# Kernel tuning notes

Hardware: AMD Instinct MI355X
Metric: run time of the kernel (lower is better)

## Reference

```python
import jax, jax.numpy as jnp
import numpy as np
from jax import lax

KS = 3
N = KS * KS  # 9 sampling locations per output pixel


def conv2d(x, w, b, pad, dil=1):
    out = lax.conv_general_dilated(
        x, w, window_strides=(1, 1), padding=((pad, pad), (pad, pad)),
        rhs_dilation=(dil, dil), dimension_numbers=('NCHW', 'OIHW', 'NCHW'))
    return out + b[None, :, None, None]


def deform_conv(x, p_w, p_b, dw, db):
    # Pure deform-conv-v2 semantics: offsets from p_conv, bilinear gather on
    # zero-padded input, then 3x3 contraction over the 9 gathered samples.
    B, C, H, W = x.shape
    offset = conv2d(x, p_w, p_b, 1)                       # (B, 2N, H, W)
    xp = jnp.pad(x, ((0, 0), (0, 0), (1, 1), (1, 1)))     # zero pad by 1
    Hp, Wp = H + 2, W + 2
    rr = jnp.arange(-(KS // 2), KS // 2 + 1)
    pi, pj = jnp.meshgrid(rr, rr, indexing='ij')
    p_n = jnp.concatenate([pi.reshape(-1), pj.reshape(-1)]).astype(x.dtype)   # (2N,)
    gi, gj = jnp.meshgrid(jnp.arange(1, H + 1), jnp.arange(1, W + 1), indexing='ij')
    p0 = jnp.concatenate([jnp.broadcast_to(gi, (N, H, W)),
                          jnp.broadcast_to(gj, (N, H, W))], 0).astype(x.dtype)  # (2N,H,W)
    p = p0[None] + p_n[None, :, None, None] + offset      # (B, 2N, H, W)
    p = jnp.transpose(p, (0, 2, 3, 1))                    # (B, H, W, 2N)
    py, px = p[..., :N], p[..., N:]
    fy, fx = jnp.floor(py), jnp.floor(px)
    lt_y = jnp.clip(fy, 0, Hp - 1); lt_x = jnp.clip(fx, 0, Wp - 1)
    rb_y = jnp.clip(fy + 1, 0, Hp - 1); rb_x = jnp.clip(fx + 1, 0, Wp - 1)
    pyc = jnp.clip(py, 0, Hp - 1); pxc = jnp.clip(px, 0, Wp - 1)
    g_lt = (1 + (lt_y - pyc)) * (1 + (lt_x - pxc))
    g_rb = (1 - (rb_y - pyc)) * (1 - (rb_x - pxc))
    g_lb = (1 + (lt_y - pyc)) * (1 - (rb_x - pxc))
    g_rt = (1 - (rb_y - pyc)) * (1 + (lt_x - pxc))
    xf = xp.reshape(B, C, Hp * Wp)

    def gather(qy, qx):
        idx = (qy.astype(jnp.int32) * Wp + qx.astype(jnp.int32)).reshape(B, -1)
        g = jax.vmap(lambda xb, ib: jnp.take(xb, ib, axis=1))(xf, idx)
        return g.reshape(B, C, H, W, N)

    x_lt = gather(lt_y, lt_x); x_rb = gather(rb_y, rb_x)
    x_lb = gather(lt_y, rb_x); x_rt = gather(rb_y, lt_x)
    samples = (g_lt[:, None] * x_lt + g_rb[:, None] * x_rb
               + g_lb[:, None] * x_lb + g_rt[:, None] * x_rt)  # (B,C,H,W,N)
    out = jnp.einsum('bchwn,ocn->bohw', samples, dw.reshape(dw.shape[0], C, N))
    return out + db[None, :, None, None]


def reference(x, w1, b1, w2, b2, w3, b3, w4, b4, p_w, p_b, dw, db, cw, cb):
    branches = [(w1, b1, 1, 1.0), (w2, b2, 3, 3.0), (w3, b3, 5, 5.0), (w4, b4, 7, 7.0)]
    feats = [deform_conv(conv2d(x, w, b, d, d) * s, p_w, p_b, dw, db)
             for (w, b, d, s) in branches]
    combined = jnp.concatenate(feats, axis=1)             # (B, 4*Cout, H, W)
    return jax.nn.relu(conv2d(combined, cw, cb, 0))


def setup_inputs() -> dict:
    B, Cin, Cout, H, W = 4, 128, 64, 128, 128
    key = jax.random.key(0)
    ks = jax.random.split(key, 16)
    sc3 = 1.0 / np.sqrt(Cin * 9)      # fan-in scale for 3x3 convs
    sc1 = 1.0 / np.sqrt(4 * Cout)     # fan-in scale for 1x1 fuse conv
    scd = 1.0 / np.sqrt(Cout * 9)     # deform main conv
    inp = {'x': jax.random.normal(ks[0], (B, Cin, H, W), jnp.float32)}
    for i in range(4):
        inp[f'w{i+1}'] = jax.random.normal(ks[1 + i], (Cout, Cin, 3, 3), jnp.float32) * sc3
        inp[f'b{i+1}'] = jax.random.normal(ks[5 + i], (Cout,), jnp.float32) * 0.01
    inp['p_w'] = jax.random.normal(ks[9], (2 * N, Cout, 3, 3), jnp.float32) * 0.01
    inp['p_b'] = jax.random.normal(ks[10], (2 * N,), jnp.float32) * 0.01
    inp['dw'] = jax.random.normal(ks[11], (Cout, Cout, 3, 3), jnp.float32) * scd
    inp['db'] = jax.random.normal(ks[12], (Cout,), jnp.float32) * 0.01
    inp['cw'] = jax.random.normal(ks[13], (Cout, 4 * Cout, 1, 1), jnp.float32) * sc1
    inp['cb'] = jax.random.normal(ks[14], (Cout,), jnp.float32) * 0.01
    return inp
```

## Files before the change

### kernel.cpp

```cpp
#include <hip/hip_runtime.h>
#include <hip/hip_fp16.h>

#define H 128
#define W 128
#define CIN 128
#define COUT 64
#define HW (H*W)
#define XW 130
#define FSL (XW*XW*64)
#define XTD 144

typedef __half f16;
typedef __attribute__((ext_vector_type(8)))  _Float16 h16x8;
typedef __attribute__((ext_vector_type(16))) float f32x16;

__device__ __forceinline__ float b2f(f16 v){ return __half2float(v); }
__device__ __forceinline__ f16  f2b(float v){ return __float2half_rn(v); }
__device__ __forceinline__ unsigned pack2(float a, float b){
    unsigned short ua = __builtin_bit_cast(unsigned short, f2b(a));
    unsigned short ub = __builtin_bit_cast(unsigned short, f2b(b));
    return (unsigned)ua | ((unsigned)ub << 16);
}
__device__ __forceinline__ unsigned short b16u(float v){
    return __builtin_bit_cast(unsigned short, f2b(v));
}
__device__ __forceinline__ __half2 uh2(unsigned u){
    return __builtin_bit_cast(__half2, u);
}
__device__ __forceinline__ unsigned h2u(__half2 v){
    return __builtin_bit_cast(unsigned, v);
}
__device__ __forceinline__ unsigned bcasth2(float v){
    __half h = __float2half_rn(v);
    return h2u(__halves2half2(h, h));
}
__device__ __forceinline__ void gld16(const void* g, void* l){
    __builtin_amdgcn_global_load_lds(
        (const __attribute__((address_space(1))) void*)g,
        (__attribute__((address_space(3))) void*)l, 16, 0, 0);
}

__global__ __launch_bounds__(256) void k_prep(
    const float* __restrict__ w1, const float* __restrict__ w2,
    const float* __restrict__ w3, const float* __restrict__ w4,
    const float* __restrict__ dw, const float* __restrict__ cw,
    const float* __restrict__ pw,
    uint4* __restrict__ xt4, unsigned* __restrict__ wbt,
    unsigned* __restrict__ dwb2, unsigned* __restrict__ cwb2,
    unsigned* __restrict__ pwb)
{
    int bid = blockIdx.x;
    int t = threadIdx.x;
    if (bid < 1024){
        const int n4 = (4*XTD*XTD*64)/4;
        for (int i = bid*256 + t; i < n4; i += 1024*256)
            xt4[i] = make_uint4(0,0,0,0);
    } else if (bid < 1600){
        int tid = (bid-1024)*256 + t;
        int cpl = tid & 7;
        int oc  = (tid >> 3) & 63;
        int tap = (tid >> 9) % 9;
        int cg  = (tid / 4608) & 7;
        int d   = tid / 36864;
        const float* wt = (d==0)?w1:(d==1)?w2:(d==2)?w3:w4;
        int c = cg*8 + cpl;
        wbt[tid] = pack2(wt[((size_t)oc*CIN + 2*c  )*9 + tap],
                         wt[((size_t)oc*CIN + 2*c+1)*9 + tap]);
    } else if (bid < 1672){
        int i = (bid-1600)*256 + t;
        int n = i>>11, oc = (i>>5)&63, cp = i&31;
        dwb2[i] = pack2(dw[((size_t)oc*64 + 2*cp  )*9 + n],
                        dw[((size_t)oc*64 + 2*cp+1)*9 + n]);
    } else if (bid < 1704){
        int i = (bid-1672)*256 + t;
        int kc = i>>9;
        int hf = (i>>8)&1;
        int oc = (i>>2)&63;
        int cl = i&3;
        int cp = kc*8 + hf*4 + cl;
        cwb2[i] = pack2(cw[(size_t)oc*256 + 2*cp], cw[(size_t)oc*256 + 2*cp+1]);
    } else {
        int i = (bid-1704)*256 + t;
        int cl = i & 3, oc = (i>>2)&31, hf = (i>>7)&1, cq = (i>>8)&3, tap = i>>10;
        int c = cq*16 + hf*8 + cl*2;
        unsigned v = 0u;
        if (oc < 18)
            v = pack2(pw[((size_t)oc*64 + c  )*9 + tap],
                      pw[((size_t)oc*64 + c+1)*9 + tap]);
        pwb[i] = v;
    }
}

__global__ __launch_bounds__(256) void k_xprep(
    const float* __restrict__ x, unsigned* __restrict__ xt)
{
    int y = blockIdx.x, b = blockIdx.y;
    int t = threadIdx.x;
    __shared__ float xsm[64*131];
    for (int ci0 = 0; ci0 < 128; ci0 += 64){
        for (int i=0;i<32;i++){
            int idx = t + 256*i;
            int col = idx & 127, ci = idx >> 7;
            xsm[ci*131 + col] = x[(((size_t)b*CIN + ci0+ci)*H + y)*W + col];
        }
        __syncthreads();
        for (int i=0;i<16;i++){
            int idx = t + 256*i;
            int cpg = idx & 31, col = idx >> 5;
            int cgg = (ci0 >> 4) + (cpg >> 3);
            int cpl = cpg & 7;
            unsigned u = pack2(xsm[(2*cpg)*131 + col], xsm[(2*cpg+1)*131 + col]);
            xt[((((size_t)b*8 + cgg)*XTD + y+8)*XTD + col+8)*8 + cpl] = u;
        }
        __syncthreads();
    }
}

__global__ __launch_bounds__(256,3) void k_branch_mfma(
    const unsigned* __restrict__ xt, const unsigned* __restrict__ wbt,
    const float* __restrict__ b1, const float* __restrict__ b2,
    const float* __restrict__ b3, const float* __restrict__ b4,
    f16* __restrict__ feats2)
{
    int bid = blockIdx.x;
    int xcd = bid & 7;
    int j   = bid >> 3;
    int zb  = xcd + 8*(j & 1);
    int hp  = j >> 1;
    int d = zb >> 2, b = zb & 3;
    int dil = 2*d + 1;
    int h0 = hp*2;
    const float* bs = (d==0)?b1:(d==1)?b2:(d==2)?b3:b4;
    const float scale = (float)dil;

    __shared__ unsigned smem[6912 + 4608];
    unsigned* As = smem;
    unsigned* Bs = smem + 6912;
    const unsigned short* As16 = (const unsigned short*)As;
    const unsigned short* Bs16 = (const unsigned short*)Bs;

    int t = threadIdx.x;
    int lane = t & 63;
    int w = t >> 6;
    int l31 = lane & 31;
    int half = lane >> 5;

    f16* fb = feats2 + (size_t)zb*FSL;
    if (t < 32){
        int yy = h0 + 1 + (t>>4);
        int side = (t>>3)&1;
        int q = t & 7;
        uint4 z = make_uint4(0,0,0,0);
        *(uint4*)((unsigned short*)fb + ((size_t)yy*XW + side*129)*64 + q*8) = z;
    }
    if (hp == 0){
        uint4 z = make_uint4(0,0,0,0);
        for (int i=t; i<2080; i+=256){
            int row = i / 1040;
            int r = i % 1040;
            int xx = r >> 3, q = r & 7;
            *(uint4*)((unsigned short*)fb + ((size_t)(row*129)*XW + xx)*64 + q*8) = z;
        }
    }

    f32x16 acc[2][2];
    #pragma unroll
    for (int i=0;i<2;i++)
      #pragma unroll
      for (int jj=0;jj<2;jj++)
        #pragma unroll
        for (int e=0;e<16;e++) acc[i][jj][e] = 0.f;

    const unsigned* xtb_b = xt + (size_t)b*8*XTD*XTD*8;
    int r = w >> 1;
    int pxb = (w & 1) * 64;

    for (int cg=0; cg<8; cg++){
        const unsigned* xs_cg = xtb_b + (size_t)cg*XTD*XTD*8;
        #pragma unroll
        for (int i=0;i<7;i++){
            int idx4 = t + 256*i;
            if (idx4 < 1728){
                int row6 = idx4 / 288;
                int rem  = idx4 - row6*288;
                int hf   = rem / 144;
                int s    = rem - hf*144;
                int ky = row6 >> 1, rr = row6 & 1;
                int yy = h0 + rr + (ky-1)*dil + 8;
                gld16(xs_cg + ((size_t)yy*XTD + (s + 8 - dil))*8 + hf*4,
                      &As[idx4*4]);
            }
        }
        const unsigned* wb_cg = wbt + ((size_t)d*8 + cg)*4608;
        #pragma unroll
        for (int i=0;i<5;i++){
            int idx4 = t + 256*i;
            if (idx4 < 1152){
                int tap = idx4 >> 7;
                int hf  = (idx4 >> 6) & 1;
                int oc  = idx4 & 63;
                gld16(wb_cg + ((size_t)tap*64 + oc)*8 + hf*4,
                      &Bs[idx4*4]);
            }
        }
        __syncthreads();
        #pragma unroll
        for (int tap=0; tap<9; tap++){
            int ky = tap/3, kx = tap%3;
            int arow = ((ky*2 + r)*2 + half)*144;
            int brow = (tap*2 + half)*64;
            h16x8 a0  = *(const h16x8*)(As16 + (arow + pxb      + l31 + kx*dil)*8);
            h16x8 a1  = *(const h16x8*)(As16 + (arow + pxb + 32 + l31 + kx*dil)*8);
            h16x8 bb0 = *(const h16x8*)(Bs16 + (brow      + l31)*8);
            h16x8 bb1 = *(const h16x8*)(Bs16 + (brow + 32 + l31)*8);
            acc[0][0] = __builtin_amdgcn_mfma_f32_32x32x16_f16(a0, bb0, acc[0][0], 0,0,0);
            acc[0][1] = __builtin_amdgcn_mfma_f32_32x32x16_f16(a0, bb1, acc[0][1], 0,0,0);
            acc[1][0] = __builtin_amdgcn_mfma_f32_32x32x16_f16(a1, bb0, acc[1][0], 0,0,0);
            acc[1][1] = __builtin_amdgcn_mfma_f32_32x32x16_f16(a1, bb1, acc[1][1], 0,0,0);
        }
        __syncthreads();
    }

    unsigned short* ep = (unsigned short*)smem;
    float bias0 = bs[l31], bias1 = bs[32 + l31];
    #pragma unroll
    for (int i=0;i<2;i++){
      #pragma unroll
      for (int jj=0;jj<2;jj++){
        int oc = jj*32 + l31;
        float bj = jj ? bias1 : bias0;
        #pragma unroll
        for (int rg=0; rg<4; rg++){
            int m0 = 64*w + 32*i + 8*rg + 4*half;
            #pragma unroll
            for (int e=0;e<4;e++)
                ep[(m0+e)*64 + oc] = b16u((acc[i][jj][4*rg+e] + bj)*scale);
        }
      }
    }
    __syncthreads();
    {
        int row = t >> 7, pxm = t & 127;
        unsigned short* drow = (unsigned short*)fb + ((size_t)(h0+1+row)*XW + pxm + 1)*64;
        const unsigned short* srow = ep + t*64;
        #pragma unroll
        for (int q=0;q<8;q++)
            *(uint4*)(drow + q*8) = *(const uint4*)(srow + q*8);
    }
}

__global__ __launch_bounds__(256,3) void k_offset_mfma(
    const f16* __restrict__ feats2,
    const unsigned* __restrict__ pwb,
    const float* __restrict__ pb,
    f16* __restrict__ offs)
{
    int bid = blockIdx.x;
    int xcd  = bid & 7;
    int h    = (bid >> 3) & 127;
    int pass = bid >> 10;
    int zb   = xcd + 8*pass;

    int t = threadIdx.x;
    int lane = t & 63, w = t >> 6;
    int l31 = lane & 31, half = lane >> 5;

    __shared__ unsigned short xs[3120*8];

    const unsigned short* fin = (const unsigned short*)(feats2 + (size_t)zb*FSL);
    #pragma unroll
    for (int i=0; i<13; i++){
        int idx4 = t + 256*i;
        if (idx4 < 3120){
            int row = idx4 / 1040;
            int r   = idx4 - row*1040;
            int col = r >> 3, q = r & 7;
            int qsrc = q ^ (col & 7);
            gld16(fin + ((size_t)(h+row)*XW + col)*64 + qsrc*8,
                  &xs[idx4*8]);
        }
    }
    __syncthreads();

    f32x16 acc;
    #pragma unroll
    for (int e=0;e<16;e++) acc[e] = 0.f;

    int pxw = 32*w + l31;
    #pragma unroll
    for (int tap=0; tap<9; tap++){
        int ky = tap/3, kx = tap%3;
        int col = pxw + kx;
        int gbase = (ky*130 + col)*8;
        int csw = col & 7;
        const unsigned* brow = pwb + (((size_t)tap*4)*2 + half)*128 + l31*4;
        #pragma unroll
        for (int cq=0; cq<4; cq++){
            int q = cq*2 + half;
            h16x8 a  = *(const h16x8*)&xs[(gbase + (q ^ csw))*8];
            h16x8 b0 = *(const h16x8*)(brow + cq*256);
            acc = __builtin_amdgcn_mfma_f32_32x32x16_f16(a, b0, acc, 0,0,0);
        }
    }
    __syncthreads();

    unsigned short* ep = (unsigned short*)xs;
    if (l31 < 18){
        float bias = pb[l31];
        #pragma unroll
        for (int rg=0; rg<4; rg++){
            int m0 = 32*w + 4*half + 8*rg;
            #pragma unroll
            for (int e=0;e<4;e++)
                ep[l31*132 + m0+e] = b16u(acc[4*rg+e] + bias);
        }
    }
    __syncthreads();
    unsigned short* obase = (unsigned short*)(offs + (size_t)zb*18*HW) ;
    for (int i=t; i<288; i+=256){
        int oc = i >> 4, sg = i & 15;
        *(uint4*)(obase + (size_t)oc*HW + h*W + sg*8) = *(const uint4*)(ep + oc*132 + sg*8);
    }
}

__global__ __launch_bounds__(256,5) void k_deform_mfma(
    const f16* __restrict__ feats2,
    const f16* __restrict__ offs,
    const unsigned* __restrict__ dwb2,
    const float* __restrict__ db,
    f16* __restrict__ dout2)
{
    int bid = blockIdx.x;
    int xcd  = bid & 7;
    int h    = (bid >> 3) & 127;
    int pass = bid >> 10;
    int zb   = xcd + 8*pass;

    int t = threadIdx.x;
    int lane = t & 63, w = t >> 6;
    int l31 = lane & 31, half = lane >> 5;
    int pxg = t >> 3;
    int cq  = t & 7;
    int sub_w = cq >> 1;
    int hf8   = cq & 1;

    #define AROW 516
    __shared__ unsigned smem_d[8*AROW + 2304 + 1024];
    unsigned* Asu = smem_d;
    unsigned* Bsu = smem_d + 8*AROW;
    unsigned* Cd  = smem_d + 8*AROW + 2304;

    const f16* obase = offs + (size_t)zb*18*HW + h*W;
    const unsigned short* fbase = (const unsigned short*)(feats2 + (size_t)zb*FSL);

    f32x16 acc0, acc1;
    #pragma unroll
    for (int e=0;e<16;e++){ acc0[e]=0.f; acc1[e]=0.f; }

#define CLOAD(S, C0, C1) { \
    const unsigned* cp_ = Cd + ((S)*32 + pxg)*8; \
    C0 = *(const uint4*)cp_; \
    C1 = *(const uint4*)(cp_ + 4); }
#define GLOAD(C1, LT, LB, RT, RB) { \
    int dxo_ = (int)(C1).y, dyo_ = (int)(C1).z; \
    const unsigned short* fc_ = fbase + (int)(C1).x + cq*8; \
    LT = *(const uint4*)(fc_); \
    LB = *(const uint4*)(fc_ + dxo_); \
    RT = *(const uint4*)(fc_ + dyo_); \
    RB = *(const uint4*)(fc_ + dyo_ + dxo_); }
#define INTERP(S, C0, LT, LB, RT, RB) { \
    __half2 wlt_ = uh2((C0).x), wlb_ = uh2((C0).y); \
    __half2 wrt_ = uh2((C0).z), wrb_ = uh2((C0).w); \
    unsigned p0_,p1_,p2_,p3_; \
    { __half2 r_ = __hmul2(wlt_, uh2((LT).x)); r_ = __hfma2(wlb_, uh2((LB).x), r_); \
      r_ = __hfma2(wrt_, uh2((RT).x), r_); r_ = __hfma2(wrb_, uh2((RB).x), r_); p0_ = h2u(r_); } \
    { __half2 r_ = __hmul2(wlt_, uh2((LT).y)); r_ = __hfma2(wlb_, uh2((LB).y), r_); \
      r_ = __hfma2(wrt_, uh2((RT).y), r_); r_ = __hfma2(wrb_, uh2((RB).y), r_); p1_ = h2u(r_); } \
    { __half2 r_ = __hmul2(wlt_, uh2((LT).z)); r_ = __hfma2(wlb_, uh2((LB).z), r_); \
      r_ = __hfma2(wrt_, uh2((RT).z), r_); r_ = __hfma2(wrb_, uh2((RB).z), r_); p2_ = h2u(r_); } \
    { __half2 r_ = __hmul2(wlt_, uh2((LT).w)); r_ = __hfma2(wlb_, uh2((LB).w), r_); \
      r_ = __hfma2(wrt_, uh2((RT).w), r_); r_ = __hfma2(wrb_, uh2((RB).w), r_); p3_ = h2u(r_); } \
    uint4 av_; av_.x=p0_; av_.y=p1_; av_.z=p2_; av_.w=p3_; \
    *(uint4*)&Asu[(sub_w*2 + hf8)*AROW + ((S)*32 + pxg)*4] = av_; }

    for (int n=0; n<9; n++){
        const uint4* dsrc = (const uint4*)(dwb2 + n*2048);
        #pragma unroll
        for (int i=0;i<2;i++){
            int j = t + 256*i;
            int idx4 = j*4;
            int oc = idx4 >> 5, cp = idx4 & 31;
            *(uint4*)&Bsu[oc*36 + cp] = dsrc[j];
        }
        if (t < 128){
            float offy = b2f(obase[n*HW + t]);
            float offx = b2f(obase[(n+9)*HW + t]);
            float py  = (float)(h + n/3) + offy;
            float pxf = (float)(t + n%3) + offx;
            float fy = floorf(py), fx = floorf(pxf);
            float lty = fminf(fmaxf(fy,     0.f),129.f);
            float ltx = fminf(fmaxf(fx,     0.f),129.f);
            float rby = fminf(fmaxf(fy+1.f, 0.f),129.f);
            float rbx = fminf(fmaxf(fx+1.f, 0.f),129.f);
            float pyc = fminf(fmaxf(py,     0.f),129.f);
            float pxc = fminf(fmaxf(pxf,    0.f),129.f);
            float ay = 1.f + (lty-pyc), by = 1.f - (rby-pyc);
            float ax = 1.f + (ltx-pxc), bx = 1.f - (rbx-pxc);
            unsigned* cp = &Cd[t*8];
            cp[0] = bcasth2(ay*ax);
            cp[1] = bcasth2(ay*bx);
            cp[2] = bcasth2(by*ax);
            cp[3] = bcasth2(by*bx);
            cp[4] = (unsigned)(((int)lty*XW + (int)ltx)*64);
            cp[5] = (unsigned)(((int)rbx - (int)ltx)*64);
            cp[6] = (unsigned)(((int)rby - (int)lty)*XW*64);
        }
        __syncthreads();

        {
            uint4 c0a, c1a, c0b, c1b;
            uint4 LTa, LBa, RTa, RBa;
            uint4 LTb, LBb, RTb, RBb;
            CLOAD(0, c0a, c1a); GLOAD(c1a, LTa, LBa, RTa, RBa);
            CLOAD(1, c0b, c1b); GLOAD(c1b, LTb, LBb, RTb, RBb);
            INTERP(0, c0a, LTa, LBa, RTa, RBa);
            CLOAD(2, c0a, c1a); GLOAD(c1a, LTa, LBa, RTa, RBa);
            INTERP(1, c0b, LTb, LBb, RTb, RBb);
            CLOAD(3, c0b, c1b); GLOAD(c1b, LTb, LBb, RTb, RBb);
            INTERP(2, c0a, LTa, LBa, RTa, RBa);
            INTERP(3, c0b, LTb, LBb, RTb, RBb);
        }
        __syncthreads();

        const unsigned short* As16 = (const unsigned short*)Asu;
        const unsigned short* Bs16 = (const unsigned short*)Bsu;
        #pragma unroll
        for (int s=0;s<4;s++){
            h16x8 a  = *(const h16x8*)(As16 + (s*2+half)*(AROW*2) + (32*w + l31)*8);
            h16x8 b0 = *(const h16x8*)(Bs16 + (l31*36 + s*8 + half*4)*2);
            h16x8 b1 = *(const h16x8*)(Bs16 + ((32+l31)*36 + s*8 + half*4)*2);
            acc0 = __builtin_amdgcn_mfma_f32_32x32x16_f16(a, b0, acc0, 0,0,0);
            acc1 = __builtin_amdgcn_mfma_f32_32x32x16_f16(a, b1, acc1, 0,0,0);
        }
        __syncthreads();
    }
#undef CLOAD
#undef GLOAD
#undef INTERP

    unsigned short* ep = (unsigned short*)smem_d;
    #pragma unroll
    for (int nt=0; nt<2; nt++){
        int oc = nt*32 + l31;
        float bias = db[oc];
        const f32x16& A = nt ? acc1 : acc0;
        #pragma unroll
        for (int rg=0; rg<4; rg++){
            int m0 = 32*w + 4*half + 8*rg;
            #pragma unroll
            for (int e=0;e<4;e++)
                ep[(m0+e)*64 + oc] = b16u(A[4*rg+e] + bias);
        }
    }
    __syncthreads();
    uint4* dst = (uint4*)((unsigned short*)dout2 + ((size_t)zb*128 + h)*(128*64));
    #pragma unroll
    for (int i=0;i<4;i++)
        dst[t + 256*i] = ((const uint4*)ep)[t + 256*i];
    #undef AROW
}

__global__ __launch_bounds__(256,2) void k_combine_mfma(
    const f16* __restrict__ dout2,
    const unsigned* __restrict__ cwb2,
    const float* __restrict__ cb,
    float* __restrict__ out)
{
    int h = blockIdx.x, b = blockIdx.y;
    int t = threadIdx.x;
    int lane = t & 63, w = t >> 6, l31 = lane & 31, half = lane >> 5;

    __shared__ float ep2[64*132];

    f32x16 acc0, acc1;
    #pragma unroll
    for (int e=0;e<16;e++){ acc0[e]=0.f; acc1[e]=0.f; }

    const unsigned short* dbase0 = (const unsigned short*)dout2;
    const unsigned short* cb16 = (const unsigned short*)cwb2;
    size_t rowsel2 = ((size_t)b*128 + h)*128 + (32*w + l31);

    unsigned AV[64];
    #pragma unroll
    for (int kc=0; kc<16; kc++){
        *(uint4*)&AV[kc*4] = *(const uint4*)(
            dbase0 + (size_t)(kc>>2)*(4*HW*64) + rowsel2*64 + (kc&3)*16 + half*8);
    }
    #pragma unroll
    for (int kc=0; kc<16; kc++){
        h16x8 a  = __builtin_bit_cast(h16x8, *(uint4*)&AV[kc*4]);
        h16x8 b0 = *(const h16x8*)(cb16 + ((kc*2+half)*64 + l31)*8);
        h16x8 b1 = *(const h16x8*)(cb16 + ((kc*2+half)*64 + 32+l31)*8);
        acc0 = __builtin_amdgcn_mfma_f32_32x32x16_f16(a, b0, acc0, 0,0,0);
        acc1 = __builtin_amdgcn_mfma_f32_32x32x16_f16(a, b1, acc1, 0,0,0);
    }

    #pragma unroll
    for (int nt=0; nt<2; nt++){
        int oc = nt*32 + l31;
        float bias = cb[oc];
        const f32x16& A = nt ? acc1 : acc0;
        #pragma unroll
        for (int rg=0; rg<4; rg++){
            int m0 = 32*w + 4*half + 8*rg;
            #pragma unroll
            for (int e=0;e<4;e++)
                ep2[oc*132 + m0+e] = fmaxf(A[4*rg+e] + bias, 0.f);
        }
    }
    __syncthreads();
    for (int i=t; i<2048; i+=256){
        int oc = i>>5, sg = i&31;
        *(uint4*)&out[(((size_t)b*64+oc)*128 + h)*128 + sg*4] = *(const uint4*)&ep2[oc*132 + sg*4];
    }
}

extern "C" void kernel_launch(void* const* d_in, const int* in_sizes, int n_in,
                              void* d_out, int out_size, void* d_ws, size_t ws_size,
                              hipStream_t stream) {
    const float* x  = (const float*)d_in[0];
    const float* w1 = (const float*)d_in[1];
    const float* b1 = (const float*)d_in[2];
    const float* w2 = (const float*)d_in[3];
    const float* b2 = (const float*)d_in[4];
    const float* w3 = (const float*)d_in[5];
    const float* b3 = (const float*)d_in[6];
    const float* w4 = (const float*)d_in[7];
    const float* b4 = (const float*)d_in[8];
    const float* pw = (const float*)d_in[9];
    const float* pb = (const float*)d_in[10];
    const float* dw = (const float*)d_in[11];
    const float* db = (const float*)d_in[12];
    const float* cw = (const float*)d_in[13];
    const float* cb = (const float*)d_in[14];
    float* out = (float*)d_out;

    f16* feats2 = (f16*)d_ws;
    f16* offs   = feats2 + (size_t)16*FSL;
    f16* region2 = offs + (size_t)16*18*HW;
    f16* dout2  = region2;
    unsigned* xt  = (unsigned*)region2;
    unsigned* wbt = xt + (size_t)4*8*XTD*XTD*8;
    unsigned* dwb2 = (unsigned*)(dout2 + (size_t)16*128*128*64);
    unsigned* cwb2 = dwb2 + 18432;
    unsigned* pwb  = cwb2 + 8192;

    k_prep        <<<dim3(1740),    256, 0, stream>>>(w1,w2,w3,w4, dw, cw, pw,
                                                      (uint4*)xt, wbt, dwb2, cwb2, pwb);
    k_xprep       <<<dim3(128,4),   256, 0, stream>>>(x, xt);
    k_branch_mfma <<<dim3(1024),    256, 0, stream>>>(xt, wbt, b1,b2,b3,b4, feats2);
    k_offset_mfma <<<dim3(2048),    256, 0, stream>>>(feats2, pwb, pb, offs);
    k_deform_mfma <<<dim3(2048),    256, 0, stream>>>(feats2, offs, dwb2, db, dout2);
    k_combine_mfma<<<dim3(128,4),   256, 0, stream>>>(dout2, cwb2, cb, out);
}
```

Baseline: 271.2 us.

## Process two output rows per block in deform kernel to reuse weight tiles

The deform kernel now has each block handle two adjacent output rows, so the grid is halved. The per-tap weight tile loaded into shared memory is reused across both rows, and all 256 threads compute sampling coefficients instead of half of them. The cost is doubled shared memory for the A tile and coefficients, four accumulator tiles instead of two, and a lower launch-bounds occupancy target (3 blocks instead of 5), which may reduce latency hiding for the gather loads.

```diff
diff --git a/kernel.cpp b/kernel.cpp
--- a/kernel.cpp
+++ b/kernel.cpp
@@ -323,7 +323,7 @@
     }
 }
 
-__global__ __launch_bounds__(256,5) void k_deform_mfma(
+__global__ __launch_bounds__(256,3) void k_deform_mfma(
     const f16* __restrict__ feats2,
     const f16* __restrict__ offs,
     const unsigned* __restrict__ dwb2,
@@ -332,9 +332,10 @@
 {
     int bid = blockIdx.x;
     int xcd  = bid & 7;
-    int h    = (bid >> 3) & 127;
-    int pass = bid >> 10;
+    int h2   = (bid >> 3) & 63;
+    int pass = bid >> 9;
     int zb   = xcd + 8*pass;
+    int hA   = h2*2;
 
     int t = threadIdx.x;
     int lane = t & 63, w = t >> 6;
@@ -345,20 +346,24 @@
     int hf8   = cq & 1;
 
     #define AROW 516
-    __shared__ unsigned smem_d[8*AROW + 2304 + 1024];
+    __shared__ unsigned smem_d[16*AROW + 2304 + 2048];
     unsigned* Asu = smem_d;
-    unsigned* Bsu = smem_d + 8*AROW;
-    unsigned* Cd  = smem_d + 8*AROW + 2304;
-
-    const f16* obase = offs + (size_t)zb*18*HW + h*W;
+    unsigned* Bsu = smem_d + 16*AROW;
+    unsigned* Cd  = smem_d + 16*AROW + 2304;
+
+    const f16* obase = offs + (size_t)zb*18*HW;
     const unsigned short* fbase = (const unsigned short*)(feats2 + (size_t)zb*FSL);
 
-    f32x16 acc0, acc1;
-    #pragma unroll
-    for (int e=0;e<16;e++){ acc0[e]=0.f; acc1[e]=0.f; }
-
-#define CLOAD(S, C0, C1) { \
-    const unsigned* cp_ = Cd + ((S)*32 + pxg)*8; \
+    f32x16 acc[2][2];
+    #pragma unroll
+    for (int i=0;i<2;i++)
+      #pragma unroll
+      for (int jj=0;jj<2;jj++)
+        #pragma unroll
+        for (int e=0;e<16;e++) acc[i][jj][e] = 0.f;
+
+#define CLOAD(CdB, S, C0, C1) { \
+    const unsigned* cp_ = (CdB) + ((S)*32 + pxg)*8; \
     C0 = *(const uint4*)cp_; \
     C1 = *(const uint4*)(cp_ + 4); }
 #define GLOAD(C1, LT, LB, RT, RB) { \
@@ -368,7 +373,7 @@
     LB = *(const uint4*)(fc_ + dxo_); \
     RT = *(const uint4*)(fc_ + dyo_); \
     RB = *(const uint4*)(fc_ + dyo_ + dxo_); }
-#define INTERP(S, C0, LT, LB, RT, RB) { \
+#define INTERP(AsuB, S, C0, LT, LB, RT, RB) { \
     __half2 wlt_ = uh2((C0).x), wlb_ = uh2((C0).y); \
     __half2 wrt_ = uh2((C0).z), wrb_ = uh2((C0).w); \
     unsigned p0_,p1_,p2_,p3_; \
@@ -381,7 +386,7 @@
     { __half2 r_ = __hmul2(wlt_, uh2((LT).w)); r_ = __hfma2(wlb_, uh2((LB).w), r_); \
       r_ = __hfma2(wrt_, uh2((RT).w), r_); r_ = __hfma2(wrb_, uh2((RB).w), r_); p3_ = h2u(r_); } \
     uint4 av_; av_.x=p0_; av_.y=p1_; av_.z=p2_; av_.w=p3_; \
-    *(uint4*)&Asu[(sub_w*2 + hf8)*AROW + ((S)*32 + pxg)*4] = av_; }
+    *(uint4*)&(AsuB)[(sub_w*2 + hf8)*AROW + ((S)*32 + pxg)*4] = av_; }
 
     for (int n=0; n<9; n++){
         const uint4* dsrc = (const uint4*)(dwb2 + n*2048);
@@ -392,11 +397,13 @@
             int oc = idx4 >> 5, cp = idx4 & 31;
             *(uint4*)&Bsu[oc*36 + cp] = dsrc[j];
         }
-        if (t < 128){
-            float offy = b2f(obase[n*HW + t]);
-            float offx = b2f(obase[(n+9)*HW + t]);
-            float py  = (float)(h + n/3) + offy;
-            float pxf = (float)(t + n%3) + offx;
+        {
+            int rr = t >> 7, px = t & 127;
+            int ht = hA + rr;
+            float offy = b2f(obase[(size_t)n*HW + ht*W + px]);
+            float offx = b2f(obase[(size_t)(n+9)*HW + ht*W + px]);
+            float py  = (float)(ht + n/3) + offy;
+            float pxf = (float)(px + n%3) + offx;
             float fy = floorf(py), fx = floorf(pxf);
             float lty = fminf(fmaxf(fy,     0.f),129.f);
             float ltx = fminf(fmaxf(fx,     0.f),129.f);
@@ -406,7 +413,7 @@
             float pxc = fminf(fmaxf(pxf,    0.f),129.f);
             float ay = 1.f + (lty-pyc), by = 1.f - (rby-pyc);
             float ax = 1.f + (ltx-pxc), bx = 1.f - (rbx-pxc);
-            unsigned* cp = &Cd[t*8];
+            unsigned* cp = &Cd[(rr*128 + px)*8];
             cp[0] = bcasth2(ay*ax);
             cp[1] = bcasth2(ay*bx);
             cp[2] = bcasth2(by*ax);
@@ -417,30 +424,36 @@
         }
         __syncthreads();
 
-        {
+        #pragma unroll
+        for (int rr=0; rr<2; rr++){
+            unsigned* CdB  = Cd  + rr*1024;
+            unsigned* AsuB = Asu + rr*8*AROW;
             uint4 c0a, c1a, c0b, c1b;
             uint4 LTa, LBa, RTa, RBa;
             uint4 LTb, LBb, RTb, RBb;
-            CLOAD(0, c0a, c1a); GLOAD(c1a, LTa, LBa, RTa, RBa);
-            CLOAD(1, c0b, c1b); GLOAD(c1b, LTb, LBb, RTb, RBb);
-            INTERP(0, c0a, LTa, LBa, RTa, RBa);
-            CLOAD(2, c0a, c1a); GLOAD(c1a, LTa, LBa, RTa, RBa);
-            INTERP(1, c0b, LTb, LBb, RTb, RBb);
-            CLOAD(3, c0b, c1b); GLOAD(c1b, LTb, LBb, RTb, RBb);
-            INTERP(2, c0a, LTa, LBa, RTa, RBa);
-            INTERP(3, c0b, LTb, LBb, RTb, RBb);
-        }
-        __syncthreads();
-
-        const unsigned short* As16 = (const unsigned short*)Asu;
+            CLOAD(CdB, 0, c0a, c1a); GLOAD(c1a, LTa, LBa, RTa, RBa);
+            CLOAD(CdB, 1, c0b, c1b); GLOAD(c1b, LTb, LBb, RTb, RBb);
+            INTERP(AsuB, 0, c0a, LTa, LBa, RTa, RBa);
+            CLOAD(CdB, 2, c0a, c1a); GLOAD(c1a, LTa, LBa, RTa, RBa);
+            INTERP(AsuB, 1, c0b, LTb, LBb, RTb, RBb);
+            CLOAD(CdB, 3, c0b, c1b); GLOAD(c1b, LTb, LBb, RTb, RBb);
+            INTERP(AsuB, 2, c0a, LTa, LBa, RTa, RBa);
+            INTERP(AsuB, 3, c0b, LTb, LBb, RTb, RBb);
+        }
+        __syncthreads();
+
         const unsigned short* Bs16 = (const unsigned short*)Bsu;
         #pragma unroll
-        for (int s=0;s<4;s++){
-            h16x8 a  = *(const h16x8*)(As16 + (s*2+half)*(AROW*2) + (32*w + l31)*8);
-            h16x8 b0 = *(const h16x8*)(Bs16 + (l31*36 + s*8 + half*4)*2);
-            h16x8 b1 = *(const h16x8*)(Bs16 + ((32+l31)*36 + s*8 + half*4)*2);
-            acc0 = __builtin_amdgcn_mfma_f32_32x32x16_f16(a, b0, acc0, 0,0,0);
-            acc1 = __builtin_amdgcn_mfma_f32_32x32x16_f16(a, b1, acc1, 0,0,0);
+        for (int rr=0; rr<2; rr++){
+            const unsigned short* As16 = (const unsigned short*)(Asu + rr*8*AROW);
+            #pragma unroll
+            for (int s=0;s<4;s++){
+                h16x8 a  = *(const h16x8*)(As16 + (s*2+half)*(AROW*2) + (32*w + l31)*8);
+                h16x8 b0 = *(const h16x8*)(Bs16 + (l31*36 + s*8 + half*4)*2);
+                h16x8 b1 = *(const h16x8*)(Bs16 + ((32+l31)*36 + s*8 + half*4)*2);
+                acc[rr][0] = __builtin_amdgcn_mfma_f32_32x32x16_f16(a, b0, acc[rr][0], 0,0,0);
+                acc[rr][1] = __builtin_amdgcn_mfma_f32_32x32x16_f16(a, b1, acc[rr][1], 0,0,0);
+            }
         }
         __syncthreads();
     }
@@ -450,22 +463,25 @@
 
     unsigned short* ep = (unsigned short*)smem_d;
     #pragma unroll
-    for (int nt=0; nt<2; nt++){
-        int oc = nt*32 + l31;
-        float bias = db[oc];
-        const f32x16& A = nt ? acc1 : acc0;
-        #pragma unroll
-        for (int rg=0; rg<4; rg++){
-            int m0 = 32*w + 4*half + 8*rg;
+    for (int rr=0; rr<2; rr++){
+        #pragma unroll
+        for (int nt=0; nt<2; nt++){
+            int oc = nt*32 + l31;
+            float bias = db[oc];
+            const f32x16& A = acc[rr][nt];
             #pragma unroll
-            for (int e=0;e<4;e++)
-                ep[(m0+e)*64 + oc] = b16u(A[4*rg+e] + bias);
+            for (int rg=0; rg<4; rg++){
+                int m0 = 32*w + 4*half + 8*rg;
+                #pragma unroll
+                for (int e=0;e<4;e++)
+                    ep[rr*8192 + (m0+e)*64 + oc] = b16u(A[4*rg+e] + bias);
+            }
         }
     }
     __syncthreads();
-    uint4* dst = (uint4*)((unsigned short*)dout2 + ((size_t)zb*128 + h)*(128*64));
-    #pragma unroll
-    for (int i=0;i<4;i++)
+    uint4* dst = (uint4*)((unsigned short*)dout2 + ((size_t)zb*128 + hA)*(128*64));
+    #pragma unroll
+    for (int i=0;i<8;i++)
         dst[t + 256*i] = ((const uint4*)ep)[t + 256*i];
     #undef AROW
 }
@@ -560,6 +576,6 @@
     k_xprep       <<<dim3(128,4),   256, 0, stream>>>(x, xt);
     k_branch_mfma <<<dim3(1024),    256, 0, stream>>>(xt, wbt, b1,b2,b3,b4, feats2);
     k_offset_mfma <<<dim3(2048),    256, 0, stream>>>(feats2, pwb, pb, offs);
-    k_deform_mfma <<<dim3(2048),    256, 0, stream>>>(feats2, offs, dwb2, db, dout2);
+    k_deform_mfma <<<dim3(1024),    256, 0, stream>>>(feats2, offs, dwb2, db, dout2);
     k_combine_mfma<<<dim3(128,4),   256, 0, stream>>>(dout2, cwb2, cb, out);
 }
```

Result: slower. 279.1 us (+2.9%).
